# Kernel tuning notes

Hardware: AMD Instinct MI355X
Metric: run time of the kernel (lower is better)

The kernel has to match this reference:

```python
import jax, jax.numpy as jnp
import numpy as np

B, S, H, D = 4, 2048, 8, 64  # batch, seq, heads, per-head dim (dim=64)
EPS = 1e-5


def _layernorm(h, g, b):
    m = jnp.mean(h, axis=-1, keepdims=True)
    v = jnp.mean(jnp.square(h - m), axis=-1, keepdims=True)
    return (h - m) * jax.lax.rsqrt(v + EPS) * g + b


def setup_inputs() -> dict:
    key = jax.random.key(0)
    ks = jax.random.split(key, 12)
    s = 1.0 / np.sqrt(D)
    return {
        "x": jax.random.normal(ks[0], (B, S, H, D), dtype=jnp.float32),
        "ln1_g": jnp.ones((D,), jnp.float32),
        "ln1_b": jnp.zeros((D,), jnp.float32),
        "Wp": jax.random.normal(ks[1], (D, 3 * D), jnp.float32) * s,
        "bp": jnp.zeros((3 * D,), jnp.float32),
        "ln2_g": jnp.ones((D,), jnp.float32),
        "ln2_b": jnp.zeros((D,), jnp.float32),
        "W1": jax.random.normal(ks[2], (D, 4 * D), jnp.float32) * s,
        "b1": jnp.zeros((4 * D,), jnp.float32),
        "W2": jax.random.normal(ks[3], (4 * D, D), jnp.float32) * (1.0 / np.sqrt(4 * D)),
        "b2": jnp.zeros((D,), jnp.float32),
    }


def reference(x, ln1_g, ln1_b, Wp, bp, ln2_g, ln2_b, W1, b1, W2, b2):
    # x: [B, S, H, D]
    h = _layernorm(x, ln1_g, ln1_b)
    qkv = h @ Wp + bp                       # [B,S,H,3D]  (dropout = identity, eval)
    q, k, v = jnp.split(qkv, 3, axis=-1)
    q = q.transpose(0, 2, 1, 3)             # [B,H,S,D]
    k = k.transpose(0, 2, 1, 3)
    v = v.transpose(0, 2, 1, 3)
    sim = jnp.einsum('bhqd,bhkd->bhqk', q, k)   # no sqrt(d) scaling (faithful)
    attn = jax.nn.softmax(sim, axis=-1)
    out = jnp.einsum('bhqk,bhkd->bhqd', attn, v).transpose(0, 2, 1, 3)  # [B,S,H,D]
    out = _layernorm(out, ln2_g, ln2_b)
    out = jax.nn.gelu(out @ W1 + b1, approximate=False) @ W2 + b2
    return out + x
```

## Files before the change

kernel.cpp:

```cpp
#include <hip/hip_runtime.h>
#include <hip/hip_bf16.h>
#include <math.h>

#define BB 4
#define SS 2048
#define HH 8
#define DD 64
#define EPSV 1e-5f

typedef __attribute__((ext_vector_type(8))) short short8;
typedef __attribute__((ext_vector_type(4))) float f32x4;
typedef __attribute__((ext_vector_type(4))) unsigned int uint4v;
typedef unsigned short ushort_t;
#define MFMA16 __builtin_amdgcn_mfma_f32_16x16x32_bf16

__device__ inline unsigned short f2bf(float f) {
    unsigned u = __builtin_bit_cast(unsigned, f);
    unsigned r = (u + 0x7fffu + ((u >> 16) & 1u)) >> 16;
    return (unsigned short)r;
}
__device__ inline float bf2f(unsigned short h) {
    unsigned u = ((unsigned)h) << 16;
    return __builtin_bit_cast(float, u);
}
__device__ inline unsigned pkbf(float a, float b) {
    __hip_bfloat162 h2 = __float22bfloat162_rn(make_float2(a, b));
    unsigned u;
    __builtin_memcpy(&u, &h2, 4);
    return u;
}

__global__ __launch_bounds__(256) void k1_ln_qkv(
    const float* __restrict__ x, const float* __restrict__ g1, const float* __restrict__ b1v,
    const float* __restrict__ Wp, const float* __restrict__ bp,
    float* __restrict__ qws, ushort_t* __restrict__ khws, ushort_t* __restrict__ vtws)
{
    __shared__ __align__(16) ushort_t Hh[64 * 72];
    __shared__ __align__(16) ushort_t Hl[64 * 72];
    __shared__ __align__(16) ushort_t Vt[64 * 72];

    const int tid = threadIdx.x;
    const int wv  = tid >> 6;
    const int lane = tid & 63;
    const int l15 = lane & 15;
    const int g   = lane >> 4;
    const int bh  = blockIdx.x & 31;
    const int sc  = blockIdx.x >> 5;
    const int b   = bh >> 3, hh = bh & 7;
    const int s0  = sc * 64;

    short8 bqh[2], bql[2], bkh[2], bkl[2], bvh[2];
    {
        const int nq = wv * 16 + l15;
        #pragma unroll
        for (int kh = 0; kh < 2; ++kh) {
            const int koff = kh * 32 + g * 8;
            #pragma unroll
            for (int j = 0; j < 8; ++j) {
                const float* wrow = Wp + (size_t)(koff + j) * 192 + nq;
                float wq = wrow[0];
                ushort_t hq = f2bf(wq);
                bqh[kh][j] = (short)hq;
                bql[kh][j] = (short)f2bf(wq - bf2f(hq));
                float wk = wrow[64];
                ushort_t hk = f2bf(wk);
                bkh[kh][j] = (short)hk;
                bkl[kh][j] = (short)f2bf(wk - bf2f(hk));
                bvh[kh][j] = (short)f2bf(wrow[128]);
            }
        }
    }
    const float biasq = bp[wv * 16 + l15];
    const float biask = bp[64 + wv * 16 + l15];
    const float biasv = bp[128 + wv * 16 + l15];

    {
        const int srow = s0 + wv * 16 + l15;
        const float* xr = x + ((size_t)(b * 2048 + srow) * 8 + hh) * 64;
        float hvv[16];
        #pragma unroll
        for (int kh = 0; kh < 2; ++kh) {
            float4 p0 = *(const float4*)(xr + kh * 32 + g * 8);
            float4 p1 = *(const float4*)(xr + kh * 32 + g * 8 + 4);
            hvv[kh*8+0]=p0.x; hvv[kh*8+1]=p0.y; hvv[kh*8+2]=p0.z; hvv[kh*8+3]=p0.w;
            hvv[kh*8+4]=p1.x; hvv[kh*8+5]=p1.y; hvv[kh*8+6]=p1.z; hvv[kh*8+7]=p1.w;
        }
        float s1 = 0.0f;
        #pragma unroll
        for (int i = 0; i < 16; ++i) s1 += hvv[i];
        s1 += __shfl_xor(s1, 16, 64);
        s1 += __shfl_xor(s1, 32, 64);
        float mean = s1 * (1.0f / 64.0f);
        float s2 = 0.0f;
        #pragma unroll
        for (int i = 0; i < 16; ++i) { float d = hvv[i] - mean; s2 += d * d; }
        s2 += __shfl_xor(s2, 16, 64);
        s2 += __shfl_xor(s2, 32, 64);
        float rstd = rsqrtf(s2 * (1.0f / 64.0f) + EPSV);

        #pragma unroll
        for (int kh = 0; kh < 2; ++kh) {
            ushort_t hi[8]; unsigned lo2[4];
            float hf[8];
            #pragma unroll
            for (int j = 0; j < 8; ++j) {
                int dI = kh * 32 + g * 8 + j;
                hf[j] = (hvv[kh*8+j] - mean) * rstd * g1[dI] + b1v[dI];
                hi[j] = f2bf(hf[j]);
            }
            uint4 HHv;
            HHv.x = (unsigned)hi[0] | ((unsigned)hi[1] << 16);
            HHv.y = (unsigned)hi[2] | ((unsigned)hi[3] << 16);
            HHv.z = (unsigned)hi[4] | ((unsigned)hi[5] << 16);
            HHv.w = (unsigned)hi[6] | ((unsigned)hi[7] << 16);
            #pragma unroll
            for (int j = 0; j < 4; ++j)
                lo2[j] = pkbf(hf[2*j] - bf2f(hi[2*j]), hf[2*j+1] - bf2f(hi[2*j+1]));
            uint4 HLv; HLv.x = lo2[0]; HLv.y = lo2[1]; HLv.z = lo2[2]; HLv.w = lo2[3];
            int off = (wv * 16 + l15) * 72 + kh * 32 + g * 8;
            *(uint4*)(&Hh[off]) = HHv;
            *(uint4*)(&Hl[off]) = HLv;
        }
    }
    __syncthreads();

    #pragma unroll
    for (int mt = 0; mt < 4; ++mt) {
        short8 ah[2], al[2];
        int abase = (mt * 16 + l15) * 72 + g * 8;
        ah[0] = *(const short8*)(&Hh[abase]);
        ah[1] = *(const short8*)(&Hh[abase + 32]);
        al[0] = *(const short8*)(&Hl[abase]);
        al[1] = *(const short8*)(&Hl[abase + 32]);

        f32x4 aq = (f32x4){0.f,0.f,0.f,0.f};
        f32x4 ak = (f32x4){0.f,0.f,0.f,0.f};
        f32x4 av = (f32x4){0.f,0.f,0.f,0.f};
        #pragma unroll
        for (int kh = 0; kh < 2; ++kh) {
            aq = MFMA16(ah[kh], bqh[kh], aq, 0, 0, 0);
            aq = MFMA16(al[kh], bqh[kh], aq, 0, 0, 0);
            aq = MFMA16(ah[kh], bql[kh], aq, 0, 0, 0);
            ak = MFMA16(ah[kh], bkh[kh], ak, 0, 0, 0);
            ak = MFMA16(al[kh], bkh[kh], ak, 0, 0, 0);
            ak = MFMA16(ah[kh], bkl[kh], ak, 0, 0, 0);
            av = MFMA16(ah[kh], bvh[kh], av, 0, 0, 0);
        }

        size_t base = ((size_t)bh * 2048 + s0 + mt * 16 + 4 * g) * 64 + wv * 16 + l15;
        #pragma unroll
        for (int r = 0; r < 4; ++r) {
            qws[base + (size_t)r * 64] = aq[r] + biasq;
            khws[base + (size_t)r * 64] = f2bf(ak[r] + biask);
        }
        uint2 vvp;
        vvp.x = pkbf(av[0] + biasv, av[1] + biasv);
        vvp.y = pkbf(av[2] + biasv, av[3] + biasv);
        *(uint2*)(&Vt[(wv * 16 + l15) * 72 + mt * 16 + 4 * g]) = vvp;
    }
    __syncthreads();

    #pragma unroll
    for (int p = 0; p < 2; ++p) {
        int slot = tid + 256 * p;
        int dd = slot >> 3, cc = slot & 7;
        int c0 = ((cc >> 2) << 5) + ((cc & 3) << 2);
        uint2 a = *(const uint2*)(&Vt[dd * 72 + c0]);
        uint2 b2 = *(const uint2*)(&Vt[dd * 72 + c0 + 16]);
        uint4 o; o.x = a.x; o.y = a.y; o.z = b2.x; o.w = b2.y;
        *(uint4*)(vtws + ((size_t)bh * 64 + dd) * 2048 + s0 + cc * 8) = o;
    }
}

#define NKT 32

__global__ __launch_bounds__(256, 2) void k2_attn(
    const float* __restrict__ qws, const ushort_t* __restrict__ khws,
    const ushort_t* __restrict__ vtws, float* __restrict__ ows)
{
    __shared__ __align__(16) ushort_t KhL[2][64 * 64];
    __shared__ __align__(16) ushort_t VtL[2][64 * 64];
    __shared__ __align__(16) ushort_t PadL[11264];

    const int tid  = threadIdx.x;
    const int w    = tid >> 6;
    const int lane = tid & 63;
    const int l15  = lane & 15;
    const int g    = lane >> 4;
    const int bh   = blockIdx.x & 31;
    const int qb0  = (blockIdx.x >> 5) * 128;

    PadL[tid] = (ushort_t)tid;
    if (blockIdx.x == 0xFFFFFFFFu) {
        ows[tid] = (float)PadL[255 - tid];
        return;
    }

    const float LOG2E = 1.4426950408889634f;
    short8 qh[2][2], ql[2][2];
    #pragma unroll
    for (int sub = 0; sub < 2; ++sub) {
        const float* qp = qws + ((size_t)bh * SS + qb0 + w * 32 + sub * 16 + l15) * 64;
        #pragma unroll
        for (int kh = 0; kh < 2; ++kh) {
            const float* p = qp + 32 * kh + 8 * g;
            #pragma unroll
            for (int j = 0; j < 8; ++j) {
                float f = p[j] * LOG2E;
                ushort_t hi = f2bf(f);
                qh[sub][kh][j] = (short)hi;
                ql[sub][kh][j] = (short)f2bf(f - bf2f(hi));
            }
        }
    }

    float lrow[2] = {0.0f, 0.0f};
    f32x4 oacc[2][4];
    #pragma unroll
    for (int sub = 0; sub < 2; ++sub)
        #pragma unroll
        for (int dt = 0; dt < 4; ++dt) oacc[sub][dt] = (f32x4){0.f, 0.f, 0.f, 0.f};

    const size_t kbase = (size_t)bh * SS * 64;
    const size_t vbase = (size_t)bh * 64 * 2048;

    const int dlo  = lane >> 3;
    const int j8   = ((lane & 7) ^ dlo) << 3;
    const int row0 = w * 8 + dlo;
    const int row1 = 32 + row0;
    const int lb0  = (64 * w) * 8;
    const int lb1  = (256 + 64 * w) * 8;

    #define K2_STAGE(buf, tg)                                                   \
        do {                                                                     \
            __builtin_amdgcn_global_load_lds(                                    \
                (const __attribute__((address_space(1))) void*)                  \
                    (khws + kbase + (size_t)((tg) * 64 + row0) * 64 + j8),       \
                (__attribute__((address_space(3))) void*)(&KhL[(buf)][lb0]),     \
                16, 0, 0);                                                       \
            __builtin_amdgcn_global_load_lds(                                    \
                (const __attribute__((address_space(1))) void*)                  \
                    (khws + kbase + (size_t)((tg) * 64 + row1) * 64 + j8),       \
                (__attribute__((address_space(3))) void*)(&KhL[(buf)][lb1]),     \
                16, 0, 0);                                                       \
            __builtin_amdgcn_global_load_lds(                                    \
                (const __attribute__((address_space(1))) void*)                  \
                    (vtws + vbase + (size_t)row0 * 2048 + (tg) * 64 + j8),       \
                (__attribute__((address_space(3))) void*)(&VtL[(buf)][lb0]),     \
                16, 0, 0);                                                       \
            __builtin_amdgcn_global_load_lds(                                    \
                (const __attribute__((address_space(1))) void*)                  \
                    (vtws + vbase + (size_t)row1 * 2048 + (tg) * 64 + j8),       \
                (__attribute__((address_space(3))) void*)(&VtL[(buf)][lb1]),     \
                16, 0, 0);                                                       \
        } while (0)

    K2_STAGE(0, 0);

    const int rsw = l15 & 7;

    for (int kt = 0; kt < NKT; ++kt) {
        __syncthreads();
        const int cur = kt & 1;

        if (kt < NKT - 1) K2_STAGE(cur ^ 1, kt + 1);

        #pragma unroll
        for (int half = 0; half < 2; ++half) {
            uint2 pA[2], pB[2];
            #pragma unroll
            for (int nf2 = 0; nf2 < 2; ++nf2) {
                const int nf = half * 2 + nf2;
                f32x4 aA = (f32x4){0.f, 0.f, 0.f, 0.f};
                f32x4 aB = (f32x4){0.f, 0.f, 0.f, 0.f};
                #pragma unroll
                for (int kh = 0; kh < 2; ++kh) {
                    short8 kah = *(const short8*)(
                        &KhL[cur][(nf * 16 + l15) * 64 + (((4 * kh + g) ^ rsw) << 3)]);
                    aA = MFMA16(kah, qh[0][kh], aA, 0, 0, 0);
                    aA = MFMA16(kah, ql[0][kh], aA, 0, 0, 0);
                    aB = MFMA16(kah, qh[1][kh], aB, 0, 0, 0);
                    aB = MFMA16(kah, ql[1][kh], aB, 0, 0, 0);
                }
                {
                    float p0 = __builtin_amdgcn_exp2f(aA[0]);
                    float p1 = __builtin_amdgcn_exp2f(aA[1]);
                    float p2 = __builtin_amdgcn_exp2f(aA[2]);
                    float p3 = __builtin_amdgcn_exp2f(aA[3]);
                    lrow[0] += (p0 + p1) + (p2 + p3);
                    pA[nf2].x = pkbf(p0, p1); pA[nf2].y = pkbf(p2, p3);
                }
                {
                    float p0 = __builtin_amdgcn_exp2f(aB[0]);
                    float p1 = __builtin_amdgcn_exp2f(aB[1]);
                    float p2 = __builtin_amdgcn_exp2f(aB[2]);
                    float p3 = __builtin_amdgcn_exp2f(aB[3]);
                    lrow[1] += (p0 + p1) + (p2 + p3);
                    pB[nf2].x = pkbf(p0, p1); pB[nf2].y = pkbf(p2, p3);
                }
            }
            short8 paA = __builtin_bit_cast(short8, (uint4v){pA[0].x, pA[0].y, pA[1].x, pA[1].y});
            short8 paB = __builtin_bit_cast(short8, (uint4v){pB[0].x, pB[0].y, pB[1].x, pB[1].y});
            #pragma unroll
            for (int dt = 0; dt < 4; ++dt) {
                short8 vbf = *(const short8*)(
                    &VtL[cur][(16 * dt + l15) * 64 + (((4 * half + g) ^ rsw) << 3)]);
                oacc[0][dt] = MFMA16(paA, vbf, oacc[0][dt], 0, 0, 0);
                oacc[1][dt] = MFMA16(paB, vbf, oacc[1][dt], 0, 0, 0);
            }
        }
    }

    #pragma unroll
    for (int sub = 0; sub < 2; ++sub) {
        float l = lrow[sub];
        l += __shfl_xor(l, 16, 64);
        l += __shfl_xor(l, 32, 64);
        float il = 1.0f / l;
        #pragma unroll
        for (int r = 0; r < 4; ++r) {
            float ilr = __shfl(il, 4 * g + r, 64);
            int row = qb0 + w * 32 + sub * 16 + 4 * g + r;
            #pragma unroll
            for (int dt = 0; dt < 4; ++dt)
                ows[((size_t)bh * SS + row) * 64 + dt * 16 + l15] = oacc[sub][dt][r] * ilr;
        }
    }
    #undef K2_STAGE
}

#define ITERS 4

__global__ __launch_bounds__(256) void k3_ln_mlp(
    const float* __restrict__ ows, const float* __restrict__ x,
    const float* __restrict__ g2, const float* __restrict__ b2v,
    const float* __restrict__ W1, const float* __restrict__ b1m,
    const float* __restrict__ W2, const float* __restrict__ b2o,
    float* __restrict__ out)
{
    __shared__ __align__(16) ushort_t Hs[16 * 264];
    __shared__ __align__(16) float Rs[4 * 16 * 72];

    const int tid  = threadIdx.x;
    const int wv   = tid >> 6;
    const int lane = tid & 63;
    const int l15  = lane & 15;
    const int g    = lane >> 4;

    short8 w1f[4][2], w2f[4][2];
    float  b1r[4][4];
    #pragma unroll
    for (int t = 0; t < 4; ++t) {
        #pragma unroll
        for (int kh = 0; kh < 2; ++kh) {
            #pragma unroll
            for (int j = 0; j < 8; ++j) {
                w1f[t][kh][j] = (short)f2bf(
                    W1[(size_t)(kh * 32 + g * 8 + j) * 256 + wv * 64 + t * 16 + l15]);
                w2f[t][kh][j] = (short)f2bf(
                    W2[(size_t)(wv * 64 + kh * 32 + g * 8 + j) * 64 + t * 16 + l15]);
            }
        }
        #pragma unroll
        for (int r = 0; r < 4; ++r)
            b1r[t][r] = b1m[wv * 64 + t * 16 + 4 * g + r];
    }

    for (int it = 0; it < ITERS; ++it) {
        const int r0 = (blockIdx.x * ITERS + it) * 16;

        const float* orow = ows + (size_t)(r0 + l15) * 64;
        float hvv[16];
        #pragma unroll
        for (int kh = 0; kh < 2; ++kh) {
            float4 p0 = *(const float4*)(orow + kh * 32 + g * 8);
            float4 p1 = *(const float4*)(orow + kh * 32 + g * 8 + 4);
            hvv[kh*8+0]=p0.x; hvv[kh*8+1]=p0.y; hvv[kh*8+2]=p0.z; hvv[kh*8+3]=p0.w;
            hvv[kh*8+4]=p1.x; hvv[kh*8+5]=p1.y; hvv[kh*8+6]=p1.z; hvv[kh*8+7]=p1.w;
        }
        float s1 = 0.0f;
        #pragma unroll
        for (int i = 0; i < 16; ++i) s1 += hvv[i];
        s1 += __shfl_xor(s1, 16, 64);
        s1 += __shfl_xor(s1, 32, 64);
        float mean = s1 * (1.0f / 64.0f);
        float s2 = 0.0f;
        #pragma unroll
        for (int i = 0; i < 16; ++i) { float d = hvv[i] - mean; s2 += d * d; }
        s2 += __shfl_xor(s2, 16, 64);
        s2 += __shfl_xor(s2, 32, 64);
        float rstd = rsqrtf(s2 * (1.0f / 64.0f) + EPSV);

        short8 h2f[2];
        #pragma unroll
        for (int kh = 0; kh < 2; ++kh) {
            float4 ga = *(const float4*)(g2 + kh * 32 + g * 8);
            float4 gb = *(const float4*)(g2 + kh * 32 + g * 8 + 4);
            float4 ba = *(const float4*)(b2v + kh * 32 + g * 8);
            float4 bb = *(const float4*)(b2v + kh * 32 + g * 8 + 4);
            float gg[8] = {ga.x,ga.y,ga.z,ga.w,gb.x,gb.y,gb.z,gb.w};
            float bv[8] = {ba.x,ba.y,ba.z,ba.w,bb.x,bb.y,bb.z,bb.w};
            #pragma unroll
            for (int j = 0; j < 8; ++j)
                h2f[kh][j] = (short)f2bf((hvv[kh*8+j] - mean) * rstd * gg[j] + bv[j]);
        }

        #pragma unroll
        for (int t = 0; t < 4; ++t) {
            f32x4 acc = (f32x4){0.f, 0.f, 0.f, 0.f};
            acc = MFMA16(w1f[t][0], h2f[0], acc, 0, 0, 0);
            acc = MFMA16(w1f[t][1], h2f[1], acc, 0, 0, 0);
            float ge[4];
            #pragma unroll
            for (int r = 0; r < 4; ++r) {
                float v = acc[r] + b1r[t][r];
                ge[r] = 0.5f * v * (1.0f + erff(v * 0.70710678118654752f));
            }
            uint2 pk;
            pk.x = pkbf(ge[0], ge[1]);
            pk.y = pkbf(ge[2], ge[3]);
            *(uint2*)(&Hs[l15 * 264 + wv * 64 + t * 16 + 4 * g]) = pk;
        }

        short8 ha[2];
        ha[0] = *(const short8*)(&Hs[l15 * 264 + wv * 64 + g * 8]);
        ha[1] = *(const short8*)(&Hs[l15 * 264 + wv * 64 + 32 + g * 8]);
        #pragma unroll
        for (int t = 0; t < 4; ++t) {
            f32x4 a2 = (f32x4){0.f, 0.f, 0.f, 0.f};
            a2 = MFMA16(ha[0], w2f[t][0], a2, 0, 0, 0);
            a2 = MFMA16(ha[1], w2f[t][1], a2, 0, 0, 0);
            #pragma unroll
            for (int r = 0; r < 4; ++r)
                Rs[wv * 1152 + (4 * g + r) * 72 + t * 16 + l15] = a2[r];
        }
        __syncthreads();

        {
            int m = tid >> 4, d4 = tid & 15;
            const float* rp = Rs + m * 72 + d4 * 4;
            f32x4 v0 = *(const f32x4*)(rp);
            f32x4 v1 = *(const f32x4*)(rp + 1152);
            f32x4 v2 = *(const f32x4*)(rp + 2304);
            f32x4 v3 = *(const f32x4*)(rp + 3456);
            f32x4 sum = v0 + v1 + v2 + v3;
            int r = r0 + m;
            int bq = r >> 14, hq = (r >> 11) & 7, sq = r & 2047;
            size_t oidx = ((size_t)(bq * 2048 + sq) * 8 + hq) * 64 + d4 * 4;
            float4 xv = *(const float4*)(x + oidx);
            float4 bo = *(const float4*)(b2o + d4 * 4);
            float4 res = make_float4(sum[0] + xv.x + bo.x, sum[1] + xv.y + bo.y,
                                     sum[2] + xv.z + bo.z, sum[3] + xv.w + bo.w);
            *(float4*)(out + oidx) = res;
        }
        __syncthreads();
    }
}

extern "C" void kernel_launch(void* const* d_in, const int* in_sizes, int n_in,
                              void* d_out, int out_size, void* d_ws, size_t ws_size,
                              hipStream_t stream) {
    const float* x     = (const float*)d_in[0];
    const float* ln1_g = (const float*)d_in[1];
    const float* ln1_b = (const float*)d_in[2];
    const float* Wp    = (const float*)d_in[3];
    const float* bp    = (const float*)d_in[4];
    const float* ln2_g = (const float*)d_in[5];
    const float* ln2_b = (const float*)d_in[6];
    const float* W1    = (const float*)d_in[7];
    const float* b1    = (const float*)d_in[8];
    const float* W2    = (const float*)d_in[9];
    const float* b2    = (const float*)d_in[10];
    float* out = (float*)d_out;

    float* ws  = (float*)d_ws;
    float* qws = ws;
    float* ows = ws + 4194304;
    ushort_t* khws = (ushort_t*)(ws + 8388608);
    ushort_t* vtws = khws + 4194304;

    k1_ln_qkv<<<dim3(1024), dim3(256), 0, stream>>>(
        x, ln1_g, ln1_b, Wp, bp, qws, khws, vtws);
    k2_attn<<<dim3(512), dim3(256), 0, stream>>>(qws, khws, vtws, ows);
    k3_ln_mlp<<<dim3(BB * HH * SS / 16 / ITERS), dim3(256), 0, stream>>>(
        ows, x, ln2_g, ln2_b, W1, b1, W2, b2, out);
}
```

Measured before the change: 177.9 us.

## Restructure LN2 across waves, use fast erf GELU, pad LDS to cap occupancy

In k3, each wave now layer-normalizes its own 16 rows of a 64-row tile into a shared bf16 buffer, and the four waves then reuse those rows across four MLP sub-tiles. Before, each wave redundantly normalized the same 16 rows on every iteration. The libm erff GELU is replaced with an Abramowitz–Stegun polynomial that uses the hardware rcp and exp2 builtins, which trades a little accuracy for fewer instructions. Both k1 and k3 get launch_bounds(256,2) and large dummy LDS arrays, kept alive by an impossible branch, which appear meant to limit blocks per CU and cut cache or LDS contention. The padding wastes LDS and may lower latency hiding.

```diff
diff --git a/kernel.cpp b/kernel.cpp
--- a/kernel.cpp
+++ b/kernel.cpp
@@ -29,8 +29,19 @@
     __builtin_memcpy(&u, &h2, 4);
     return u;
 }
-
-__global__ __launch_bounds__(256) void k1_ln_qkv(
+__device__ inline float gelu_f(float v) {
+    float a = v * 0.70710678118654752f;
+    float z = fabsf(a);
+    float t = __builtin_amdgcn_rcpf(fmaf(0.3275911f, z, 1.0f));
+    float p = t * fmaf(t, fmaf(t, fmaf(t, fmaf(t, 1.061405429f, -1.453152027f),
+                                       1.421413741f), -0.284496736f), 0.254829592f);
+    float e = __builtin_amdgcn_exp2f(-z * z * 1.4426950408889634f);
+    float erfz = fmaf(-p, e, 1.0f);
+    float se = (a < 0.0f) ? -erfz : erfz;
+    return 0.5f * v * (1.0f + se);
+}
+
+__global__ __launch_bounds__(256, 2) void k1_ln_qkv(
     const float* __restrict__ x, const float* __restrict__ g1, const float* __restrict__ b1v,
     const float* __restrict__ Wp, const float* __restrict__ bp,
     float* __restrict__ qws, ushort_t* __restrict__ khws, ushort_t* __restrict__ vtws)
@@ -38,6 +49,7 @@
     __shared__ __align__(16) ushort_t Hh[64 * 72];
     __shared__ __align__(16) ushort_t Hl[64 * 72];
     __shared__ __align__(16) ushort_t Vt[64 * 72];
+    __shared__ __align__(16) ushort_t PadK1[13824];
 
     const int tid = threadIdx.x;
     const int wv  = tid >> 6;
@@ -48,6 +60,12 @@
     const int sc  = blockIdx.x >> 5;
     const int b   = bh >> 3, hh = bh & 7;
     const int s0  = sc * 64;
+
+    PadK1[tid] = (ushort_t)tid;
+    if (blockIdx.x == 0xFFFFFFFFu) {
+        qws[tid] = (float)PadK1[255 - tid];
+        return;
+    }
 
     short8 bqh[2], bql[2], bkh[2], bkl[2], bvh[2];
     {
@@ -329,17 +347,17 @@
     #undef K2_STAGE
 }
 
-#define ITERS 4
-
-__global__ __launch_bounds__(256) void k3_ln_mlp(
+__global__ __launch_bounds__(256, 2) void k3_ln_mlp(
     const float* __restrict__ ows, const float* __restrict__ x,
     const float* __restrict__ g2, const float* __restrict__ b2v,
     const float* __restrict__ W1, const float* __restrict__ b1m,
     const float* __restrict__ W2, const float* __restrict__ b2o,
     float* __restrict__ out)
 {
+    __shared__ __align__(16) ushort_t Hb[64 * 72];
     __shared__ __align__(16) ushort_t Hs[16 * 264];
     __shared__ __align__(16) float Rs[4 * 16 * 72];
+    __shared__ __align__(16) ushort_t PadK3[9600];
 
     const int tid  = threadIdx.x;
     const int wv   = tid >> 6;
@@ -347,6 +365,12 @@
     const int l15  = lane & 15;
     const int g    = lane >> 4;
 
+    PadK3[tid] = (ushort_t)tid;
+    if (blockIdx.x == 0xFFFFFFFFu) {
+        out[tid] = (float)PadK3[255 - tid];
+        return;
+    }
+
     short8 w1f[4][2], w2f[4][2];
     float  b1r[4][4];
     #pragma unroll
@@ -366,10 +390,10 @@
             b1r[t][r] = b1m[wv * 64 + t * 16 + 4 * g + r];
     }
 
-    for (int it = 0; it < ITERS; ++it) {
-        const int r0 = (blockIdx.x * ITERS + it) * 16;
-
-        const float* orow = ows + (size_t)(r0 + l15) * 64;
+    const int r0 = blockIdx.x * 64;
+
+    {
+        const float* orow = ows + (size_t)(r0 + wv * 16 + l15) * 64;
         float hvv[16];
         #pragma unroll
         for (int kh = 0; kh < 2; ++kh) {
@@ -391,19 +415,28 @@
         s2 += __shfl_xor(s2, 32, 64);
         float rstd = rsqrtf(s2 * (1.0f / 64.0f) + EPSV);
 
+        #pragma unroll
+        for (int kh = 0; kh < 2; ++kh) {
+            ushort_t hi[8];
+            #pragma unroll
+            for (int j = 0; j < 8; ++j) {
+                int dI = kh * 32 + g * 8 + j;
+                hi[j] = f2bf((hvv[kh*8+j] - mean) * rstd * g2[dI] + b2v[dI]);
+            }
+            uint4 HHv;
+            HHv.x = (unsigned)hi[0] | ((unsigned)hi[1] << 16);
+            HHv.y = (unsigned)hi[2] | ((unsigned)hi[3] << 16);
+            HHv.z = (unsigned)hi[4] | ((unsigned)hi[5] << 16);
+            HHv.w = (unsigned)hi[6] | ((unsigned)hi[7] << 16);
+            *(uint4*)(&Hb[(wv * 16 + l15) * 72 + kh * 32 + g * 8]) = HHv;
+        }
+    }
+    __syncthreads();
+
+    for (int mt = 0; mt < 4; ++mt) {
         short8 h2f[2];
-        #pragma unroll
-        for (int kh = 0; kh < 2; ++kh) {
-            float4 ga = *(const float4*)(g2 + kh * 32 + g * 8);
-            float4 gb = *(const float4*)(g2 + kh * 32 + g * 8 + 4);
-            float4 ba = *(const float4*)(b2v + kh * 32 + g * 8);
-            float4 bb = *(const float4*)(b2v + kh * 32 + g * 8 + 4);
-            float gg[8] = {ga.x,ga.y,ga.z,ga.w,gb.x,gb.y,gb.z,gb.w};
-            float bv[8] = {ba.x,ba.y,ba.z,ba.w,bb.x,bb.y,bb.z,bb.w};
-            #pragma unroll
-            for (int j = 0; j < 8; ++j)
-                h2f[kh][j] = (short)f2bf((hvv[kh*8+j] - mean) * rstd * gg[j] + bv[j]);
-        }
+        h2f[0] = *(const short8*)(&Hb[(mt * 16 + l15) * 72 + g * 8]);
+        h2f[1] = *(const short8*)(&Hb[(mt * 16 + l15) * 72 + 32 + g * 8]);
 
         #pragma unroll
         for (int t = 0; t < 4; ++t) {
@@ -412,10 +445,8 @@
             acc = MFMA16(w1f[t][1], h2f[1], acc, 0, 0, 0);
             float ge[4];
             #pragma unroll
-            for (int r = 0; r < 4; ++r) {
-                float v = acc[r] + b1r[t][r];
-                ge[r] = 0.5f * v * (1.0f + erff(v * 0.70710678118654752f));
-            }
+            for (int r = 0; r < 4; ++r)
+                ge[r] = gelu_f(acc[r] + b1r[t][r]);
             uint2 pk;
             pk.x = pkbf(ge[0], ge[1]);
             pk.y = pkbf(ge[2], ge[3]);
@@ -444,7 +475,7 @@
             f32x4 v2 = *(const f32x4*)(rp + 2304);
             f32x4 v3 = *(const f32x4*)(rp + 3456);
             f32x4 sum = v0 + v1 + v2 + v3;
-            int r = r0 + m;
+            int r = r0 + mt * 16 + m;
             int bq = r >> 14, hq = (r >> 11) & 7, sq = r & 2047;
             size_t oidx = ((size_t)(bq * 2048 + sq) * 8 + hq) * 64 + d4 * 4;
             float4 xv = *(const float4*)(x + oidx);
@@ -482,6 +513,6 @@
     k1_ln_qkv<<<dim3(1024), dim3(256), 0, stream>>>(
         x, ln1_g, ln1_b, Wp, bp, qws, khws, vtws);
     k2_attn<<<dim3(512), dim3(256), 0, stream>>>(qws, khws, vtws, ows);
-    k3_ln_mlp<<<dim3(BB * HH * SS / 16 / ITERS), dim3(256), 0, stream>>>(
+    k3_ln_mlp<<<dim3(1024), dim3(256), 0, stream>>>(
         ows, x, ln2_g, ln2_b, W1, b1, W2, b2, out);
 }
```

Measured after the change: 168.5 us. 1.06x faster.
